# Performance work log

Measured on AMD Instinct MI355X. Metric: run time of the kernel, lower is better.

## Reference

```python
import jax, jax.numpy as jnp
import numpy as np

EMB = 512
HID = 512
NCLASS = 50257
BATCH = 64
STEPS = 256


def setup_inputs() -> dict:
    key = jax.random.key(0)
    ks = jax.random.split(key, 14)
    s_e = 1.0 / np.sqrt(EMB)
    s_h = 1.0 / np.sqrt(HID)
    inp = {
        "X": jax.random.randint(ks[0], (BATCH, STEPS), 0, NCLASS, dtype=jnp.int32),
        "emb": jax.random.normal(ks[1], (NCLASS, EMB), jnp.float32) * 0.02,
        # layer 1: gates concatenated in order [i, f, g, o]
        "Wi": jax.random.normal(ks[2], (EMB, 4 * HID), jnp.float32) * s_e,
        "Wh": jax.random.normal(ks[3], (HID, 4 * HID), jnp.float32) * s_h,
        "bi": jax.random.normal(ks[4], (4 * HID,), jnp.float32) * 0.01,
        "bh": jax.random.normal(ks[5], (4 * HID,), jnp.float32) * 0.01,
        # layer 2 (computed but unused for the output, as in the original)
        "Wi1": jax.random.normal(ks[6], (HID, 4 * HID), jnp.float32) * s_h,
        "Wh1": jax.random.normal(ks[7], (HID, 4 * HID), jnp.float32) * s_h,
        "bi1": jax.random.normal(ks[8], (4 * HID,), jnp.float32) * 0.01,
        "bh1": jax.random.normal(ks[9], (4 * HID,), jnp.float32) * 0.01,
        # output projection (nn.Linear(n_hidden, n_class, bias=False) => W: [n_class, n_hidden])
        "Wout": jax.random.normal(ks[10], (NCLASS, HID), jnp.float32) * s_h,
        "bout": jnp.ones((NCLASS,), jnp.float32),
    }
    return inp


def _gates(pre):
    i, f, g, o = jnp.split(pre, 4, axis=-1)
    return jax.nn.sigmoid(i), jax.nn.sigmoid(f), jnp.tanh(g), jax.nn.sigmoid(o)


def reference(X, emb, Wi, Wh, bi, bh, Wi1, Wh1, bi1, bh1, Wout, bout):
    x = emb[X]  # [B, T, E]
    B = x.shape[0]
    # precompute input projections for layer 1 for all timesteps: [T, B, 4H]
    xw = jnp.einsum("bte,eh->tbh", x, Wi) + bi + bh

    h0 = jnp.zeros((B, HID), x.dtype)
    carry0 = (h0, h0, h0, h0)  # h, c, h1, c1

    def step(carry, xw_t):
        h, c, h1, c1 = carry
        i, f, g, o = _gates(xw_t + h @ Wh)
        c = f * c + i * g
        h = o * jnp.tanh(c)
        i1, f1, g1, o1 = _gates(h @ Wi1 + bi1 + h1 @ Wh1 + bh1)
        c1 = f1 * c1 + i1 * g1
        h1 = o1 * jnp.tanh(c1)
        return (h, c, h1, c1), None

    (h, c, h1, c1), _ = jax.lax.scan(step, carry0, xw)
    # original: outputs[-1] is layer-1 h at the last timestep
    return h @ Wout.T + bout
```

## Files before the change

### kernel.cpp

```cpp
#include <hip/hip_runtime.h>
#include <cstdint>
#include <cstddef>

#define EMB    512
#define HID    512
#define NCLASS 50257
#define BATCH  64
#define STEPS  256
#define FOURH  2048

typedef __attribute__((ext_vector_type(8))) short    bf16x8;
typedef __attribute__((ext_vector_type(4))) float    f32x4;
typedef __attribute__((ext_vector_type(8))) _Float16 h8v;

__device__ __forceinline__ unsigned short f2bf(float f) {
    union { float f; unsigned int u; } v; v.f = f;
    unsigned int u = v.u;
    return (unsigned short)((u + 0x7fffu + ((u >> 16) & 1u)) >> 16);
}


__global__ void k_bias(const float* __restrict__ bi, const float* __restrict__ bh,
                       float* __restrict__ bias) {
    int i = blockIdx.x * 256 + threadIdx.x;
    if (i < FOURH) bias[i] = bi[i] + bh[i];
}

__global__ void k_wit(const float* __restrict__ Wi, unsigned short* __restrict__ WiT) {
    int n = blockIdx.x;
    int l = threadIdx.x;
    int k0 = l * 8;
    unsigned short t[8];
#pragma unroll
    for (int i = 0; i < 8; i++)
        t[i] = f2bf(Wi[(size_t)(k0 + i) * FOURH + n]);
    uint4 v;
    v.x = (unsigned)t[0] | ((unsigned)t[1] << 16);
    v.y = (unsigned)t[2] | ((unsigned)t[3] << 16);
    v.z = (unsigned)t[4] | ((unsigned)t[5] << 16);
    v.w = (unsigned)t[6] | ((unsigned)t[7] << 16);
    *(uint4*)(WiT + (size_t)n * EMB + k0) = v;
}

__global__ void k_whP(const float* __restrict__ Wh, _Float16* __restrict__ WhP) {
    int idx = blockIdx.x;
    int bidb = idx >> 5, c = idx & 31;
    int ul   = ((c >> 4) << 2) + ((c >> 2) & 3);
    int gate = c & 3;
    int gcol = gate * 512 + bidb * 8 + ul;
    int k0 = threadIdx.x * 8;
    h8v r;
#pragma unroll
    for (int i = 0; i < 8; i++)
        r[i] = (_Float16)Wh[(size_t)(k0 + i) * FOURH + gcol];
    *(h8v*)(WhP + (size_t)idx * 512 + k0) = r;
}

__global__ void k_gather(const int* __restrict__ X, const float* __restrict__ emb,
                         unsigned short* __restrict__ XA) {
    int chunk = blockIdx.x * 256 + threadIdx.x;
    int m  = chunk >> 6;
    int c8 = (chunk & 63) * 8;
    int t = m >> 6, b = m & 63;
    int row = X[b * STEPS + t];
    const float4* src = (const float4*)(emb + (size_t)row * EMB + c8);
    float4 f0 = src[0], f1 = src[1];
    uint4 v;
    v.x = (unsigned)f2bf(f0.x) | ((unsigned)f2bf(f0.y) << 16);
    v.y = (unsigned)f2bf(f0.z) | ((unsigned)f2bf(f0.w) << 16);
    v.z = (unsigned)f2bf(f1.x) | ((unsigned)f2bf(f1.y) << 16);
    v.w = (unsigned)f2bf(f1.z) | ((unsigned)f2bf(f1.w) << 16);
    *(uint4*)(XA + (size_t)m * EMB + c8) = v;
}

__global__ void k_zero(int* __restrict__ p, int n) {
    int i = blockIdx.x * 256 + threadIdx.x;
    if (i < n) p[i] = 0;
}

__global__ __launch_bounds__(256) void k_gemm1(const unsigned short* __restrict__ XA,
                                               const unsigned short* __restrict__ WiT,
                                               const float* __restrict__ bias,
                                               float* __restrict__ XWT) {
    __shared__ unsigned short Al[64 * 48];
    __shared__ unsigned short Bl[64 * 48];
    const int t  = blockIdx.y;
    const int m0 = t * 64;
    const int n0 = blockIdx.x * 64;
    const int tid  = threadIdx.x;
    const int w    = tid >> 6;
    const int lane = tid & 63;
    const int quad = lane >> 4;
    const int l16  = lane & 15;
    const int ar = tid >> 2;
    const int ac = (tid & 3) * 8;

    f32x4 acc[4];
#pragma unroll
    for (int i = 0; i < 4; i++) acc[i] = (f32x4){0.f, 0.f, 0.f, 0.f};

    for (int kk = 0; kk < 16; kk++) {
        const int k0 = kk * 32;
        __syncthreads();
        *(uint4*)(&Al[ar * 48 + ac]) = *(const uint4*)(XA  + (size_t)(m0 + ar) * EMB + k0 + ac);
        *(uint4*)(&Bl[ar * 48 + ac]) = *(const uint4*)(WiT + (size_t)(n0 + ar) * EMB + k0 + ac);
        __syncthreads();
        bf16x8 afrag = *(const bf16x8*)(&Bl[(w * 16 + l16) * 48 + quad * 8]);
#pragma unroll
        for (int mt = 0; mt < 4; mt++) {
            bf16x8 bfrag = *(const bf16x8*)(&Al[(mt * 16 + l16) * 48 + quad * 8]);
            acc[mt] = __builtin_amdgcn_mfma_f32_16x16x32_bf16(afrag, bfrag, acc[mt], 0, 0, 0);
        }
    }
    float bv[4];
#pragma unroll
    for (int r = 0; r < 4; r++) bv[r] = bias[n0 + w * 16 + quad * 4 + r];
#pragma unroll
    for (int mt = 0; mt < 4; mt++)
#pragma unroll
        for (int r = 0; r < 4; r++)
            XWT[((size_t)t * FOURH + n0 + w * 16 + quad * 4 + r) * 64 + mt * 16 + l16]
                = acc[mt][r] + bv[r];
}

__global__ __launch_bounds__(512, 1) void k_rnn(const float* __restrict__ XWT,
                                                const _Float16* __restrict__ WhP,
                                                _Float16* __restrict__ hG,
                                                float* __restrict__ hfinal,
                                                unsigned int* __restrict__ flags) {
    __shared__ _Float16 hw[64 * 8];
    __shared__ unsigned wcnt;

    const int tid  = threadIdx.x;
    const int bid  = blockIdx.x;
    const int lane = tid & 63;
    const int wid  = tid >> 6;
    const int quad = lane >> 4;
    const int l16  = lane & 15;
    const int ct   = wid >> 2;
    const int bt   = wid & 3;
    const int u    = ct * 4 + quad;
    const int b    = bt * 16 + l16;

    if (tid == 0) wcnt = 0;
    __syncthreads();

    h8v afrag[16];
    const _Float16* wsrc = WhP + ((size_t)(bid * 32 + ct * 16 + l16)) * 512 + quad * 8;
#pragma unroll
    for (int kk = 0; kk < 16; kk++) afrag[kk] = *(const h8v*)(wsrc + kk * 32);

    float c_state = 0.f;
    const size_t xwoff = (size_t)(bid * 8 + u) * 64 + b;

    float xw0, xw1, xw2, xw3;
    {
        const float* xp = XWT + xwoff;
        xw0 = xp[0]; xw1 = xp[32768]; xw2 = xp[65536]; xw3 = xp[98304];
    }

    for (int t = 0; t < STEPS; t++) {
        {
            const unsigned tgt = (unsigned)t;
            unsigned guard = 0;
            unsigned v = __hip_atomic_load(&flags[lane * 16],
                                           __ATOMIC_RELAXED, __HIP_MEMORY_SCOPE_AGENT);
            while (!__all(v >= tgt)) {
                __builtin_amdgcn_s_sleep(1);
                if (++guard > (1u << 17)) break;
                v = __hip_atomic_load(&flags[lane * 16],
                                      __ATOMIC_RELAXED, __HIP_MEMORY_SCOPE_AGENT);
            }
        }

        const char* hsrc = (const char*)hG + (size_t)(t & 1) * 65536
                         + (size_t)b * 1024 + quad * 16;
        uint4 qv[16];
#pragma unroll
        for (int kk = 0; kk < 16; kk++)
            asm volatile("global_load_dwordx4 %0, %1, off sc0 sc1"
                         : "=v"(qv[kk]) : "v"(hsrc + kk * 64));
        asm volatile("s_waitcnt vmcnt(0)" ::: "memory");
        __builtin_amdgcn_sched_barrier(0);

        f32x4 acc0 = {0.f, 0.f, 0.f, 0.f};
        f32x4 acc1 = {0.f, 0.f, 0.f, 0.f};
#pragma unroll
        for (int kk = 0; kk < 16; kk += 2) {
            union { uint4 q; h8v v; } f0, f1;
            f0.q = qv[kk]; f1.q = qv[kk + 1];
            acc0 = __builtin_amdgcn_mfma_f32_16x16x32_f16(afrag[kk],     f0.v, acc0, 0, 0, 0);
            acc1 = __builtin_amdgcn_mfma_f32_16x16x32_f16(afrag[kk + 1], f1.v, acc1, 0, 0, 0);
        }
        f32x4 acc = acc0 + acc1;

        float pre0 = acc[0] + xw0;
        float pre1 = acc[1] + xw1;
        float pre2 = acc[2] + xw2;
        float pre3 = acc[3] + xw3;
        float is = 1.f / (1.f + __expf(-pre0));
        float fs = 1.f / (1.f + __expf(-pre1));
        float gt = tanhf(pre2);
        float os = 1.f / (1.f + __expf(-pre3));
        c_state = fs * c_state + is * gt;
        float hnew = os * tanhf(c_state);

        if (t == STEPS - 1) {
            hfinal[(size_t)b * HID + bid * 8 + u] = hnew;
            break;
        }

        hw[b * 8 + u] = (_Float16)hnew;
        asm volatile("s_waitcnt lgkmcnt(0)" ::: "memory");
        if (quad == 0) {
            unsigned long long g = *(const unsigned long long*)(hw + b * 8 + ct * 4);
            unsigned long long* dst = (unsigned long long*)((char*)hG
                + (size_t)((t + 1) & 1) * 65536 + (size_t)b * 1024 + bid * 16 + ct * 8);
            __hip_atomic_store(dst, g, __ATOMIC_RELAXED, __HIP_MEMORY_SCOPE_AGENT);
        }
        asm volatile("s_waitcnt vmcnt(0)" ::: "memory");
        if (lane == 0) {
            unsigned old = atomicAdd(&wcnt, 1u);
            if (old == (unsigned)(8 * t + 7))
                __hip_atomic_store(&flags[bid * 16], (unsigned)(t + 1),
                                   __ATOMIC_RELAXED, __HIP_MEMORY_SCOPE_AGENT);
        }

        {
            const float* xp = XWT + (size_t)(t + 1) * (FOURH * 64) + xwoff;
            xw0 = xp[0]; xw1 = xp[32768]; xw2 = xp[65536]; xw3 = xp[98304];
            asm volatile("" :: "v"(xw0), "v"(xw1), "v"(xw2), "v"(xw3));
        }
    }
}

__global__ __launch_bounds__(128) void k_out(const float* __restrict__ Wout,
                                             const float* __restrict__ bout,
                                             const float* __restrict__ hfinal,
                                             float* __restrict__ out) {
    __shared__ float hl[BATCH * 128];
    const int tid = threadIdx.x;
    const int n = blockIdx.x * 128 + tid;
    const bool valid = n < NCLASS;
    float acc[BATCH];
#pragma unroll
    for (int b = 0; b < BATCH; b++) acc[b] = 0.f;
    const float4* W4 = (const float4*)Wout;
    const float4* h4 = (const float4*)hfinal;
    float4* hl4 = (float4*)hl;

    for (int kq = 0; kq < 4; kq++) {
        __syncthreads();
#pragma unroll
        for (int i = 0; i < 16; i++) {
            int f = i * 128 + tid;
            int b = f >> 5, kk = f & 31;
            hl4[f] = h4[b * 128 + kq * 32 + kk];
        }
        __syncthreads();
        if (valid) {
            for (int kk = 0; kk < 32; kk++) {
                float4 wv = W4[(size_t)n * 128 + kq * 32 + kk];
#pragma unroll
                for (int b = 0; b < BATCH; b++) {
                    float4 hv = hl4[b * 32 + kk];
                    acc[b] = fmaf(wv.x, hv.x, acc[b]);
                    acc[b] = fmaf(wv.y, hv.y, acc[b]);
                    acc[b] = fmaf(wv.z, hv.z, acc[b]);
                    acc[b] = fmaf(wv.w, hv.w, acc[b]);
                }
            }
        }
    }
    if (valid) {
        float bv = bout[n];
        for (int b = 0; b < BATCH; b++)
            out[(size_t)b * NCLASS + n] = acc[b] + bv;
    }
}


extern "C" void kernel_launch(void* const* d_in, const int* in_sizes, int n_in,
                              void* d_out, int out_size, void* d_ws, size_t ws_size,
                              hipStream_t stream) {
    const int*   X    = (const int*)  d_in[0];
    const float* emb  = (const float*)d_in[1];
    const float* Wi   = (const float*)d_in[2];
    const float* Wh   = (const float*)d_in[3];
    const float* bi   = (const float*)d_in[4];
    const float* bh   = (const float*)d_in[5];
    const float* Wout = (const float*)d_in[10];
    const float* bout = (const float*)d_in[11];
    float* out = (float*)d_out;

    char* w = (char*)d_ws;
    float*          XWT    = (float*)(w);
    unsigned short* XA     = (unsigned short*)(w + 134217728);
    _Float16*       hG     = (_Float16*)(w + 150732800);
    unsigned int*   flags  = (unsigned int*)(w + 150863872);
    unsigned short* WiT    = (unsigned short*)(w + 150994944);
    _Float16*       WhP    = (_Float16*)(w + 153092096);
    float*          bias   = (float*)(w + 155189248);
    float*          hfinal = (float*)(w + 155197440);

    k_bias  <<<8,    256, 0, stream>>>(bi, bh, bias);
    k_wit   <<<2048,  64, 0, stream>>>(Wi, WiT);
    k_whP   <<<2048,  64, 0, stream>>>(Wh, WhP);
    k_gather<<<4096, 256, 0, stream>>>(X, emb, XA);
    k_gemm1 <<<dim3(32, 256), 256, 0, stream>>>(XA, WiT, bias, XWT);
    k_zero  <<<132,  256, 0, stream>>>((int*)hG, 33792);

    k_rnn   <<<64,   512, 0, stream>>>(XWT, WhP, hG, hfinal, flags);

    k_out   <<<393,  128, 0, stream>>>(Wout, bout, hfinal, out);
}
```

Measured before the change: 1.992 ms.

## Halve RNN block waves and replace per-block flags with a single global counter

Each k_rnn block now runs 4 waves instead of 8, and each wave computes both column tiles, so it keeps two sets of Wh fragments and issues twice the MFMAs per h load. This halves the redundant global h loads per block and the intra-block counter traffic. Cross-block sync switches from 64 per-block flag slots polled by a wave-wide vote to one shared counter that each block atomically increments and that waiters compare against NBLK*t. The counter reduces the poll to a single address but puts contention on one atomic, and per-wave register pressure rises from the doubled fragments and accumulators.

```diff
diff --git a/kernel.cpp b/kernel.cpp
--- a/kernel.cpp
+++ b/kernel.cpp
@@ -8,6 +8,7 @@
 #define BATCH  64
 #define STEPS  256
 #define FOURH  2048
+#define NBLK   64
 
 typedef __attribute__((ext_vector_type(8))) short    bf16x8;
 typedef __attribute__((ext_vector_type(4))) float    f32x4;
@@ -123,7 +124,7 @@
                 = acc[mt][r] + bv[r];
 }
 
-__global__ __launch_bounds__(512, 1) void k_rnn(const float* __restrict__ XWT,
+__global__ __launch_bounds__(256, 1) void k_rnn(const float* __restrict__ XWT,
                                                 const _Float16* __restrict__ WhP,
                                                 _Float16* __restrict__ hG,
                                                 float* __restrict__ hfinal,
@@ -134,42 +135,45 @@
     const int tid  = threadIdx.x;
     const int bid  = blockIdx.x;
     const int lane = tid & 63;
-    const int wid  = tid >> 6;
+    const int bt   = tid >> 6;
     const int quad = lane >> 4;
     const int l16  = lane & 15;
-    const int ct   = wid >> 2;
-    const int bt   = wid & 3;
-    const int u    = ct * 4 + quad;
     const int b    = bt * 16 + l16;
 
     if (tid == 0) wcnt = 0;
     __syncthreads();
 
-    h8v afrag[16];
-    const _Float16* wsrc = WhP + ((size_t)(bid * 32 + ct * 16 + l16)) * 512 + quad * 8;
-#pragma unroll
-    for (int kk = 0; kk < 16; kk++) afrag[kk] = *(const h8v*)(wsrc + kk * 32);
-
-    float c_state = 0.f;
-    const size_t xwoff = (size_t)(bid * 8 + u) * 64 + b;
-
-    float xw0, xw1, xw2, xw3;
-    {
-        const float* xp = XWT + xwoff;
-        xw0 = xp[0]; xw1 = xp[32768]; xw2 = xp[65536]; xw3 = xp[98304];
+    h8v afrag[2][16];
+#pragma unroll
+    for (int tt = 0; tt < 2; tt++) {
+        const _Float16* wsrc = WhP + ((size_t)(bid * 32 + tt * 16 + l16)) * 512 + quad * 8;
+#pragma unroll
+        for (int kk = 0; kk < 16; kk++) afrag[tt][kk] = *(const h8v*)(wsrc + kk * 32);
+    }
+
+    float c0 = 0.f, c1 = 0.f;
+    const size_t xwo0 = (size_t)(bid * 8 + quad) * 64 + b;
+    const size_t xwo1 = (size_t)(bid * 8 + 4 + quad) * 64 + b;
+    unsigned int* ectr = flags;
+
+    float xwA[4], xwB[4];
+#pragma unroll
+    for (int g = 0; g < 4; g++) {
+        xwA[g] = XWT[(size_t)g * 32768 + xwo0];
+        xwB[g] = XWT[(size_t)g * 32768 + xwo1];
     }
 
     for (int t = 0; t < STEPS; t++) {
         {
-            const unsigned tgt = (unsigned)t;
+            const unsigned tgt = (unsigned)(NBLK * t);
             unsigned guard = 0;
-            unsigned v = __hip_atomic_load(&flags[lane * 16],
-                                           __ATOMIC_RELAXED, __HIP_MEMORY_SCOPE_AGENT);
-            while (!__all(v >= tgt)) {
+            unsigned v = __hip_atomic_load(ectr, __ATOMIC_RELAXED,
+                                           __HIP_MEMORY_SCOPE_AGENT);
+            while (v < tgt) {
                 __builtin_amdgcn_s_sleep(1);
                 if (++guard > (1u << 17)) break;
-                v = __hip_atomic_load(&flags[lane * 16],
-                                      __ATOMIC_RELAXED, __HIP_MEMORY_SCOPE_AGENT);
+                v = __hip_atomic_load(ectr, __ATOMIC_RELAXED,
+                                      __HIP_MEMORY_SCOPE_AGENT);
             }
         }
 
@@ -183,53 +187,68 @@
         asm volatile("s_waitcnt vmcnt(0)" ::: "memory");
         __builtin_amdgcn_sched_barrier(0);
 
-        f32x4 acc0 = {0.f, 0.f, 0.f, 0.f};
-        f32x4 acc1 = {0.f, 0.f, 0.f, 0.f};
+        f32x4 aA0 = {0.f,0.f,0.f,0.f}, aA1 = {0.f,0.f,0.f,0.f};
+        f32x4 aB0 = {0.f,0.f,0.f,0.f}, aB1 = {0.f,0.f,0.f,0.f};
 #pragma unroll
         for (int kk = 0; kk < 16; kk += 2) {
             union { uint4 q; h8v v; } f0, f1;
             f0.q = qv[kk]; f1.q = qv[kk + 1];
-            acc0 = __builtin_amdgcn_mfma_f32_16x16x32_f16(afrag[kk],     f0.v, acc0, 0, 0, 0);
-            acc1 = __builtin_amdgcn_mfma_f32_16x16x32_f16(afrag[kk + 1], f1.v, acc1, 0, 0, 0);
-        }
-        f32x4 acc = acc0 + acc1;
-
-        float pre0 = acc[0] + xw0;
-        float pre1 = acc[1] + xw1;
-        float pre2 = acc[2] + xw2;
-        float pre3 = acc[3] + xw3;
-        float is = 1.f / (1.f + __expf(-pre0));
-        float fs = 1.f / (1.f + __expf(-pre1));
-        float gt = tanhf(pre2);
-        float os = 1.f / (1.f + __expf(-pre3));
-        c_state = fs * c_state + is * gt;
-        float hnew = os * tanhf(c_state);
+            aA0 = __builtin_amdgcn_mfma_f32_16x16x32_f16(afrag[0][kk],     f0.v, aA0, 0, 0, 0);
+            aB0 = __builtin_amdgcn_mfma_f32_16x16x32_f16(afrag[1][kk],     f0.v, aB0, 0, 0, 0);
+            aA1 = __builtin_amdgcn_mfma_f32_16x16x32_f16(afrag[0][kk + 1], f1.v, aA1, 0, 0, 0);
+            aB1 = __builtin_amdgcn_mfma_f32_16x16x32_f16(afrag[1][kk + 1], f1.v, aB1, 0, 0, 0);
+        }
+        f32x4 accA = aA0 + aA1;
+        f32x4 accB = aB0 + aB1;
+
+        float iA = 1.f / (1.f + __expf(-(accA[0] + xwA[0])));
+        float fA = 1.f / (1.f + __expf(-(accA[1] + xwA[1])));
+        float gA = tanhf(accA[2] + xwA[2]);
+        float oA = 1.f / (1.f + __expf(-(accA[3] + xwA[3])));
+        c0 = fA * c0 + iA * gA;
+        float hnA = oA * tanhf(c0);
+
+        float iB = 1.f / (1.f + __expf(-(accB[0] + xwB[0])));
+        float fB = 1.f / (1.f + __expf(-(accB[1] + xwB[1])));
+        float gB = tanhf(accB[2] + xwB[2]);
+        float oB = 1.f / (1.f + __expf(-(accB[3] + xwB[3])));
+        c1 = fB * c1 + iB * gB;
+        float hnB = oB * tanhf(c1);
 
         if (t == STEPS - 1) {
-            hfinal[(size_t)b * HID + bid * 8 + u] = hnew;
+            hfinal[(size_t)b * HID + bid * 8 + quad]     = hnA;
+            hfinal[(size_t)b * HID + bid * 8 + 4 + quad] = hnB;
             break;
         }
 
-        hw[b * 8 + u] = (_Float16)hnew;
+        hw[b * 8 + quad]     = (_Float16)hnA;
+        hw[b * 8 + 4 + quad] = (_Float16)hnB;
         asm volatile("s_waitcnt lgkmcnt(0)" ::: "memory");
         if (quad == 0) {
-            unsigned long long g = *(const unsigned long long*)(hw + b * 8 + ct * 4);
+            const unsigned long long* src = (const unsigned long long*)(hw + b * 8);
+            unsigned long long lo = src[0], hi = src[1];
             unsigned long long* dst = (unsigned long long*)((char*)hG
-                + (size_t)((t + 1) & 1) * 65536 + (size_t)b * 1024 + bid * 16 + ct * 8);
-            __hip_atomic_store(dst, g, __ATOMIC_RELAXED, __HIP_MEMORY_SCOPE_AGENT);
+                + (size_t)((t + 1) & 1) * 65536 + (size_t)b * 1024 + bid * 16);
+            __hip_atomic_store(dst,     lo, __ATOMIC_RELAXED, __HIP_MEMORY_SCOPE_AGENT);
+            __hip_atomic_store(dst + 1, hi, __ATOMIC_RELAXED, __HIP_MEMORY_SCOPE_AGENT);
         }
         asm volatile("s_waitcnt vmcnt(0)" ::: "memory");
         if (lane == 0) {
             unsigned old = atomicAdd(&wcnt, 1u);
-            if (old == (unsigned)(8 * t + 7))
-                __hip_atomic_store(&flags[bid * 16], (unsigned)(t + 1),
-                                   __ATOMIC_RELAXED, __HIP_MEMORY_SCOPE_AGENT);
+            if (old == (unsigned)(4 * t + 3))
+                __hip_atomic_fetch_add(ectr, 1u, __ATOMIC_RELAXED,
+                                       __HIP_MEMORY_SCOPE_AGENT);
         }
 
         {
-            const float* xp = XWT + (size_t)(t + 1) * (FOURH * 64) + xwoff;
-            xw0 = xp[0]; xw1 = xp[32768]; xw2 = xp[65536]; xw3 = xp[98304];
-            asm volatile("" :: "v"(xw0), "v"(xw1), "v"(xw2), "v"(xw3));
+            const float* xp = XWT + (size_t)(t + 1) * (FOURH * 64);
+#pragma unroll
+            for (int g = 0; g < 4; g++) {
+                xwA[g] = xp[(size_t)g * 32768 + xwo0];
+                xwB[g] = xp[(size_t)g * 32768 + xwo1];
+            }
+            asm volatile("" :: "v"(xwA[0]), "v"(xwA[1]), "v"(xwA[2]), "v"(xwA[3]),
+                              "v"(xwB[0]), "v"(xwB[1]), "v"(xwB[2]), "v"(xwB[3]));
         }
     }
 }
@@ -310,7 +329,7 @@
     k_gemm1 <<<dim3(32, 256), 256, 0, stream>>>(XA, WiT, bias, XWT);
     k_zero  <<<132,  256, 0, stream>>>((int*)hG, 33792);
 
-    k_rnn   <<<64,   512, 0, stream>>>(XWT, WhP, hG, hfinal, flags);
+    k_rnn   <<<NBLK, 256, 0, stream>>>(XWT, WhP, hG, hfinal, flags);
 
     k_out   <<<393,  128, 0, stream>>>(Wout, bout, hfinal, out);
 }
```

Result: faster. 1.877 ms (-5.8%).
